# Kernel tuning notes

Hardware: AMD Instinct MI355X
Metric: run time of the kernel (lower is better)

Reference implementation:

```python
import jax, jax.numpy as jnp
import numpy as np

ALPHA = 1.0   # alpha=1 -> loss = alpha*loss_shape; temporal term weighted by (1-alpha)=0
GAMMA = 0.01  # soft-DTW smoothing
G = 0.05      # logistic weight steepness (weighted-DTW, Jeong et al. 2011)
BIG = 1e9     # finite 'infinity' (keeps vjp NaN-free vs. true inf)


def _softdtw(D, gamma):
    # Soft-DTW value of cost matrix D [N,N] via anti-diagonal (wavefront) scan.
    # R(i,j) = D[i,j] + softmin_gamma(R(i-1,j-1), R(i-1,j), R(i,j-1)),
    # R(-1,-1)=0, other out-of-range = +inf. Diagonal k holds cells (i, k-i).
    N = D.shape[-1]
    i = jnp.arange(N)

    def step(carry, k):
        r2, r1 = carry            # diagonals k-2 and k-1, indexed by row i
        j = k - i
        valid = (j >= 0) & (j < N)
        dk = jnp.where(valid, D[i, jnp.clip(j, 0, N - 1)], 0.0)
        up = jnp.where(i > 0, jnp.roll(r1, 1), BIG)     # R(i-1, j)
        left = r1                                        # R(i, j-1) (BIG where invalid)
        dg = jnp.where(i > 0, jnp.roll(r2, 1), BIG)      # R(i-1, j-1)
        dg = jnp.where((i == 0) & (j == 0), 0.0, dg)     # R(-1,-1) = 0 boundary
        smin = -gamma * jax.nn.logsumexp(jnp.stack([-dg, -up, -left]) / gamma, axis=0)
        rk = jnp.where(valid, dk + smin, BIG)
        return (r1, rk), None

    r0 = jnp.full((N,), BIG, dtype=D.dtype)
    (_, rlast), _ = jax.lax.scan(step, (r0, r0), jnp.arange(2 * N - 1))
    return rlast[N - 1]  # cell (N-1, N-1)


def _weighted_dilate(inp, tgt):
    B, N, _ = inp.shape
    idx = jnp.arange(N, dtype=inp.dtype)
    # modified-logistic weight on |i-j|, midpoint N/2, steepness g
    w = 1.0 / (1.0 + jnp.exp(-G * (jnp.abs(idx[:, None] - idx[None, :]) - N / 2.0)))
    # pairwise squared euclidean cost: D[b,i,j] = sum_d (tgt[b,i,d]-inp[b,j,d])^2
    D = jnp.sum((tgt[:, :, None, :] - inp[:, None, :, :]) ** 2, axis=-1) * w
    sdtw = jax.vmap(lambda d: _softdtw(d, GAMMA))(D)  # [B]
    loss_shape = jnp.mean(sdtw)
    return ALPHA * loss_shape  # (1-alpha)*loss_temporal == 0 at default alpha=1


def setup_inputs() -> dict:
    key = jax.random.key(0)
    k1, k2 = jax.random.split(key)
    B, N, Dm = 32, 1024, 1
    return {
        "input": jax.random.normal(k1, (B, N, Dm), dtype=jnp.float32),
        "target": jax.random.normal(k2, (B, N, Dm), dtype=jnp.float32),
    }


def reference(input, target):
    return _weighted_dilate(input, target)
```

## Files before the change

### kernel.cpp

```cpp
#include <hip/hip_runtime.h>
#include <math.h>

#define NN 1024
#define BATCH 32
#define P 8
#define NW 4
#define THREADS 256
#define DD 32
#define SW 32
#define SPAN 160
#define NT 64
#define RB 4
#define GW 0.05f
#define K2 144.2695040888963f
#define INV_K2 0.0069314718055994531f
#define BIGS 1.4426950408889634e11f

#define EXP2F(x) __builtin_amdgcn_exp2f(x)
#define LOG2F(x) __builtin_amdgcn_logf(x)

union F2U { float2 f; unsigned long long u; };

__device__ __forceinline__ float dppshr(float oldv, float src) {
    return __int_as_float(__builtin_amdgcn_update_dpp(
        __float_as_int(oldv), __float_as_int(src), 0x138, 0xF, 0xF, false));
}

__global__ __launch_bounds__(512) void ws_init(int* __restrict__ f) {
    f[threadIdx.x] = 0;
}

__global__ __launch_bounds__(THREADS) void sdtw_pipe8(
        const float* __restrict__ inp, const float* __restrict__ tgt,
        float* __restrict__ partial, int* __restrict__ flags,
        int* __restrict__ acks, unsigned long long* __restrict__ gx)
{
    __shared__ float xs[NN];
    __shared__ float wlblk[3136];
    __shared__ float2 exch[2][SPAN];

    const int bid = blockIdx.x;
    const int b = bid & 31;
    const int p = bid >> 5;
    const int tid = threadIdx.x;
    const int w = tid >> 6;
    const int lane = tid & 63;

    for (int tdx = tid; tdx < NN; tdx += THREADS) {
        xs[tdx] = inp[b * NN + tdx];
        float mO = (float)(2 * tdx + 1) - 1023.0f;
        float mE = (float)(2 * tdx) - 1023.0f;
        wlblk[544 + tdx]        = K2 / (1.0f + __expf(-GW * (fabsf(mO) - 512.0f)));
        wlblk[544 + 1024 + tdx] = K2 / (1.0f + __expf(-GW * (fabsf(mE) - 512.0f)));
    }

    const int i = 128 * p - (DD - 1) + SW * w + lane;
    const int i0 = i - lane;
    const bool rowValid = (unsigned)i < (unsigned)NN;
    int ic = min(max(i, 0), NN - 1);
    const float ti = tgt[b * NN + ic];
    const int imask = rowValid ? i : 0x3FFFFFFF;
    const float* wpBase = &wlblk[544 + 511 - i];

    float r1 = BIGS, r2 = BIGS;
    float dgp = (i == 0) ? 0.0f : BIGS;
    float bndUp = BIGS;
    float xv = 0.0f;
    int ackC = 0;

    __syncthreads();

    const int fin = b * P + p;
    const int fout = fin + 1;
    unsigned long long* gout = gx + (size_t)fout * RB * DD;
    const unsigned long long* ginb = gx + (size_t)fin * RB * DD;

    for (int t = 0; t < NT; ++t) {
        if (w == NW - 1 && p < P - 1 && t >= RB && ackC <= t - RB) {
            ackC = __hip_atomic_load(&acks[fout], __ATOMIC_RELAXED,
                                     __HIP_MEMORY_SCOPE_AGENT);
        }

        const int kbase = t << 5;
        const float* wp = wpBase + (t << 4);
        int c = kbase - 1 - i;  c = min(max(c, 0), NN - 1);
        xv = xs[c];
        int c0 = kbase - i0;    c0 = min(max(c0, 0), NN - 1);
        const float xf0 = xs[c0];
        const int jj0 = kbase - imask;

        #pragma unroll
        for (int d = 0; d < DD; ++d) {
            xv = dppshr((d == 0) ? xf0 : xv, xv);
            const float up = dppshr((d == 0) ? bndUp : r1, r1);
            const float dg = dgp;
            const float left = r1;
            const float wv = (d & 1) ? wp[1024 + ((d + 1) >> 1)]
                                     : wp[(d >> 1)];
            const float diff = ti - xv;
            const float dk = diff * diff * wv;
            const float mn = fminf(fminf(dg, up), left);
            const float md = __builtin_amdgcn_fmed3f(dg, up, left);
            const float mx = fmaxf(fmaxf(dg, up), left);
            const float s = 1.0f + EXP2F(mn - md) + EXP2F(mn - mx);
            float r = dk + mn - LOG2F(s);
            r = (jj0 >= -d) ? r : BIGS;
            r2 = r1; r1 = r; dgp = up;
        }
        if (t == NT - 1) break;

        const int buf = t & 1;
        if (lane >= DD - 1) exch[buf][SW * w + lane] = make_float2(r1, r2);
        if (w == NW - 1 && p < P - 1) {
            if (t >= RB) {
                while (ackC < t - (RB - 1)) {
                    __builtin_amdgcn_s_sleep(1);
                    ackC = __hip_atomic_load(&acks[fout], __ATOMIC_RELAXED,
                                             __HIP_MEMORY_SCOPE_AGENT);
                }
            }
            if (lane >= DD - 1 && lane < 63) {
                F2U v; v.f = make_float2(r1, r2);
                __hip_atomic_store(&gout[(size_t)(t & (RB - 1)) * DD + (lane - (DD - 1))],
                                   v.u, __ATOMIC_RELAXED, __HIP_MEMORY_SCOPE_AGENT);
            }
            asm volatile("s_waitcnt vmcnt(0)" ::: "memory");
            if (lane == 63)
                __hip_atomic_store(&flags[fout], t + 1, __ATOMIC_RELAXED,
                                   __HIP_MEMORY_SCOPE_AGENT);
        }
        __syncthreads();
        if (w > 0) {
            if (lane < DD - 1) { float2 v = exch[buf][SW * w + lane]; r1 = v.x; r2 = v.y; }
            float2 bv = exch[buf][SW * w - 1];
            float nd = dppshr(0.0f, r2);
            if (lane == 0)           { bndUp = bv.x; dgp = bv.y; }
            else if (lane <= DD - 2) dgp = nd;
        } else if (p > 0) {
            int fl;
            do {
                fl = __hip_atomic_load(&flags[fin], __ATOMIC_RELAXED,
                                       __HIP_MEMORY_SCOPE_AGENT);
                if (fl < t + 1) __builtin_amdgcn_s_sleep(1);
            } while (fl < t + 1);
            asm volatile("" ::: "memory");
            const unsigned long long* gslot = ginb + (size_t)(t & (RB - 1)) * DD;
            if (lane < DD - 1) {
                F2U v; v.u = __hip_atomic_load((unsigned long long*)&gslot[lane + 1],
                                               __ATOMIC_RELAXED, __HIP_MEMORY_SCOPE_AGENT);
                r1 = v.f.x; r2 = v.f.y;
            }
            F2U bv; bv.f = make_float2(BIGS, BIGS);
            if (lane == 0)
                bv.u = __hip_atomic_load((unsigned long long*)&gslot[0],
                                         __ATOMIC_RELAXED, __HIP_MEMORY_SCOPE_AGENT);
            float nd = dppshr(0.0f, r2);
            if (lane == 0)           { bndUp = bv.f.x; dgp = bv.f.y; }
            else if (lane <= DD - 2) dgp = nd;
            asm volatile("s_waitcnt vmcnt(0)" ::: "memory");
            if (lane == 0)
                __hip_atomic_store(&acks[fin], t + 1, __ATOMIC_RELAXED,
                                   __HIP_MEMORY_SCOPE_AGENT);
        } else {
            bndUp = BIGS;
        }
    }

    if (i == NN - 1) partial[b] = r2 * INV_K2;
}

__global__ __launch_bounds__(64) void reduce_mean32(const float* __restrict__ partial,
                                                    float* __restrict__ out) {
    float v = (threadIdx.x < BATCH) ? partial[threadIdx.x] : 0.0f;
    #pragma unroll
    for (int off = 32; off > 0; off >>= 1) v += __shfl_down(v, off);
    if (threadIdx.x == 0) out[0] = v * (1.0f / (float)BATCH);
}

extern "C" void kernel_launch(void* const* d_in, const int* in_sizes, int n_in,
                              void* d_out, int out_size, void* d_ws, size_t ws_size,
                              hipStream_t stream) {
    const float* inp = (const float*)d_in[0];
    const float* tgt = (const float*)d_in[1];
    float* out = (float*)d_out;

    float* partial = (float*)d_ws;
    int* flags = (int*)((char*)d_ws + 128);
    int* acks  = (int*)((char*)d_ws + 128 + 1024);
    unsigned long long* gx = (unsigned long long*)((char*)d_ws + 128 + 2048);

    ws_init<<<1, 512, 0, stream>>>(flags);
    sdtw_pipe8<<<BATCH * P, THREADS, 0, stream>>>(inp, tgt, partial, flags, acks, gx);
    reduce_mean32<<<1, 64, 0, stream>>>(partial, out);
}
```

Measured before the change: 229.0 us.

## Replace flag handshake with tagged payload words and prefetched cross-block boundary loads

Removes the separate per-block flag counter and instead packs a step tag into the upper 32 bits of each exchanged 64-bit word, so the consumer polls the data itself rather than a flag followed by a data load. The consumer issues its boundary loads speculatively before the block barrier and checks the tags after it. The producer's store and ack wait move to the start of the next step, and the vmcnt drains are dropped. The barrier becomes a raw s_barrier with only an LDS wait, and the ring depth shrinks from 4 to 2. This aims to take a global round trip and a memory fence off the critical wavefront path, in exchange for twice the payload traffic, a larger zero-init kernel, and more reliance on relaxed ordering being correct.

```diff
diff --git a/kernel.cpp b/kernel.cpp
--- a/kernel.cpp
+++ b/kernel.cpp
@@ -10,7 +10,7 @@
 #define SW 32
 #define SPAN 160
 #define NT 64
-#define RB 4
+#define RB 2
 #define GW 0.05f
 #define K2 144.2695040888963f
 #define INV_K2 0.0069314718055994531f
@@ -19,21 +19,27 @@
 #define EXP2F(x) __builtin_amdgcn_exp2f(x)
 #define LOG2F(x) __builtin_amdgcn_logf(x)
 
-union F2U { float2 f; unsigned long long u; };
+typedef unsigned long long u64;
 
 __device__ __forceinline__ float dppshr(float oldv, float src) {
     return __int_as_float(__builtin_amdgcn_update_dpp(
         __float_as_int(oldv), __float_as_int(src), 0x138, 0xF, 0xF, false));
 }
 
-__global__ __launch_bounds__(512) void ws_init(int* __restrict__ f) {
-    f[threadIdx.x] = 0;
+__device__ __forceinline__ u64 pk(float v, unsigned tag) {
+    return ((u64)tag << 32) | (u64)__float_as_uint(v);
+}
+
+__global__ __launch_bounds__(256) void ws_init(int* __restrict__ acks,
+                                               u64* __restrict__ gx) {
+    if (blockIdx.x == 128) acks[threadIdx.x] = 0;
+    else gx[(size_t)blockIdx.x * 256 + threadIdx.x] = 0;
 }
 
 __global__ __launch_bounds__(THREADS) void sdtw_pipe8(
         const float* __restrict__ inp, const float* __restrict__ tgt,
-        float* __restrict__ partial, int* __restrict__ flags,
-        int* __restrict__ acks, unsigned long long* __restrict__ gx)
+        float* __restrict__ partial, int* __restrict__ acks,
+        u64* __restrict__ gx)
 {
     __shared__ float xs[NN];
     __shared__ float wlblk[3136];
@@ -72,13 +78,79 @@
 
     const int fin = b * P + p;
     const int fout = fin + 1;
-    unsigned long long* gout = gx + (size_t)fout * RB * DD;
-    const unsigned long long* ginb = gx + (size_t)fin * RB * DD;
+    u64* gout = gx + (size_t)fout * (RB * DD * 2);
+    u64* ginb = gx + (size_t)fin * (RB * DD * 2);
+
+    const bool isProd = (w == NW - 1) && (p < P - 1);
+    const bool isCons = (w == 0) && (p > 0);
+
+    u64 pfA = 0, pfB = 0, pfC0 = 0, pfC1 = 0;
 
     for (int t = 0; t < NT; ++t) {
-        if (w == NW - 1 && p < P - 1 && t >= RB && ackC <= t - RB) {
-            ackC = __hip_atomic_load(&acks[fout], __ATOMIC_RELAXED,
-                                     __HIP_MEMORY_SCOPE_AGENT);
+        if (t > 0) {
+            if (isProd) {
+                if (t > RB) {
+                    while (ackC < t - RB) {
+                        __builtin_amdgcn_s_sleep(1);
+                        ackC = __hip_atomic_load(&acks[fout], __ATOMIC_RELAXED,
+                                                 __HIP_MEMORY_SCOPE_AGENT);
+                    }
+                }
+                if (lane >= DD - 1 && lane < 63) {
+                    u64* gq = gout + (size_t)((t - 1) & (RB - 1)) * (DD * 2)
+                                   + (size_t)(lane - (DD - 1)) * 2;
+                    __hip_atomic_store(&gq[0], pk(r1, (unsigned)t),
+                                       __ATOMIC_RELAXED, __HIP_MEMORY_SCOPE_AGENT);
+                    __hip_atomic_store(&gq[1], pk(r2, (unsigned)t),
+                                       __ATOMIC_RELAXED, __HIP_MEMORY_SCOPE_AGENT);
+                }
+                ackC = __hip_atomic_load(&acks[fout], __ATOMIC_RELAXED,
+                                         __HIP_MEMORY_SCOPE_AGENT);
+            }
+            if (w > 0) {
+                const int buf = (t - 1) & 1;
+                if (lane < DD - 1) { float2 v = exch[buf][SW * w + lane]; r1 = v.x; r2 = v.y; }
+                float2 bv = exch[buf][SW * w - 1];
+                float nd = dppshr(0.0f, r2);
+                if (lane == 0)           { bndUp = bv.x; dgp = bv.y; }
+                else if (lane <= DD - 2) dgp = nd;
+            } else if (p > 0) {
+                const unsigned expect = (unsigned)t;
+                const u64* gslot = ginb + (size_t)((t - 1) & (RB - 1)) * (DD * 2);
+                for (;;) {
+                    int ok = 1;
+                    if (lane < DD - 1)
+                        ok = ((unsigned)(pfA >> 32) == expect) &
+                             ((unsigned)(pfB >> 32) == expect);
+                    if (lane == 0)
+                        ok &= ((unsigned)(pfC0 >> 32) == expect) &
+                              ((unsigned)(pfC1 >> 32) == expect);
+                    if (__all(ok)) break;
+                    if (lane < DD - 1) {
+                        pfA = __hip_atomic_load((u64*)&gslot[(size_t)(lane + 1) * 2],
+                                                __ATOMIC_RELAXED, __HIP_MEMORY_SCOPE_AGENT);
+                        pfB = __hip_atomic_load((u64*)&gslot[(size_t)(lane + 1) * 2 + 1],
+                                                __ATOMIC_RELAXED, __HIP_MEMORY_SCOPE_AGENT);
+                    }
+                    if (lane == 0) {
+                        pfC0 = __hip_atomic_load((u64*)&gslot[0],
+                                                 __ATOMIC_RELAXED, __HIP_MEMORY_SCOPE_AGENT);
+                        pfC1 = __hip_atomic_load((u64*)&gslot[1],
+                                                 __ATOMIC_RELAXED, __HIP_MEMORY_SCOPE_AGENT);
+                    }
+                }
+                if (lane < DD - 1) { r1 = __uint_as_float((unsigned)pfA);
+                                     r2 = __uint_as_float((unsigned)pfB); }
+                float nd = dppshr(0.0f, r2);
+                if (lane == 0) { bndUp = __uint_as_float((unsigned)pfC0);
+                                 dgp   = __uint_as_float((unsigned)pfC1); }
+                else if (lane <= DD - 2) dgp = nd;
+                if (lane == 0)
+                    __hip_atomic_store(&acks[fin], (int)(pfC0 >> 32),
+                                       __ATOMIC_RELAXED, __HIP_MEMORY_SCOPE_AGENT);
+            } else {
+                bndUp = BIGS;
+            }
         }
 
         const int kbase = t << 5;
@@ -109,61 +181,29 @@
         }
         if (t == NT - 1) break;
 
-        const int buf = t & 1;
-        if (lane >= DD - 1) exch[buf][SW * w + lane] = make_float2(r1, r2);
-        if (w == NW - 1 && p < P - 1) {
-            if (t >= RB) {
-                while (ackC < t - (RB - 1)) {
-                    __builtin_amdgcn_s_sleep(1);
-                    ackC = __hip_atomic_load(&acks[fout], __ATOMIC_RELAXED,
-                                             __HIP_MEMORY_SCOPE_AGENT);
-                }
-            }
-            if (lane >= DD - 1 && lane < 63) {
-                F2U v; v.f = make_float2(r1, r2);
-                __hip_atomic_store(&gout[(size_t)(t & (RB - 1)) * DD + (lane - (DD - 1))],
-                                   v.u, __ATOMIC_RELAXED, __HIP_MEMORY_SCOPE_AGENT);
-            }
-            asm volatile("s_waitcnt vmcnt(0)" ::: "memory");
-            if (lane == 63)
-                __hip_atomic_store(&flags[fout], t + 1, __ATOMIC_RELAXED,
-                                   __HIP_MEMORY_SCOPE_AGENT);
+        if (w < NW - 1 && lane >= DD - 1)
+            exch[t & 1][SW * w + lane] = make_float2(r1, r2);
+
+        if (isCons) {
+            const u64* gslot = ginb + (size_t)(t & (RB - 1)) * (DD * 2);
+            if (lane < DD - 1) {
+                pfA = __hip_atomic_load((u64*)&gslot[(size_t)(lane + 1) * 2],
+                                        __ATOMIC_RELAXED, __HIP_MEMORY_SCOPE_AGENT);
+                pfB = __hip_atomic_load((u64*)&gslot[(size_t)(lane + 1) * 2 + 1],
+                                        __ATOMIC_RELAXED, __HIP_MEMORY_SCOPE_AGENT);
+            }
+            if (lane == 0) {
+                pfC0 = __hip_atomic_load((u64*)&gslot[0],
+                                         __ATOMIC_RELAXED, __HIP_MEMORY_SCOPE_AGENT);
+                pfC1 = __hip_atomic_load((u64*)&gslot[1],
+                                         __ATOMIC_RELAXED, __HIP_MEMORY_SCOPE_AGENT);
+            }
         }
-        __syncthreads();
-        if (w > 0) {
-            if (lane < DD - 1) { float2 v = exch[buf][SW * w + lane]; r1 = v.x; r2 = v.y; }
-            float2 bv = exch[buf][SW * w - 1];
-            float nd = dppshr(0.0f, r2);
-            if (lane == 0)           { bndUp = bv.x; dgp = bv.y; }
-            else if (lane <= DD - 2) dgp = nd;
-        } else if (p > 0) {
-            int fl;
-            do {
-                fl = __hip_atomic_load(&flags[fin], __ATOMIC_RELAXED,
-                                       __HIP_MEMORY_SCOPE_AGENT);
-                if (fl < t + 1) __builtin_amdgcn_s_sleep(1);
-            } while (fl < t + 1);
-            asm volatile("" ::: "memory");
-            const unsigned long long* gslot = ginb + (size_t)(t & (RB - 1)) * DD;
-            if (lane < DD - 1) {
-                F2U v; v.u = __hip_atomic_load((unsigned long long*)&gslot[lane + 1],
-                                               __ATOMIC_RELAXED, __HIP_MEMORY_SCOPE_AGENT);
-                r1 = v.f.x; r2 = v.f.y;
-            }
-            F2U bv; bv.f = make_float2(BIGS, BIGS);
-            if (lane == 0)
-                bv.u = __hip_atomic_load((unsigned long long*)&gslot[0],
-                                         __ATOMIC_RELAXED, __HIP_MEMORY_SCOPE_AGENT);
-            float nd = dppshr(0.0f, r2);
-            if (lane == 0)           { bndUp = bv.f.x; dgp = bv.f.y; }
-            else if (lane <= DD - 2) dgp = nd;
-            asm volatile("s_waitcnt vmcnt(0)" ::: "memory");
-            if (lane == 0)
-                __hip_atomic_store(&acks[fin], t + 1, __ATOMIC_RELAXED,
-                                   __HIP_MEMORY_SCOPE_AGENT);
-        } else {
-            bndUp = BIGS;
-        }
+
+        asm volatile("s_waitcnt lgkmcnt(0)" ::: "memory");
+        __builtin_amdgcn_s_barrier();
+        asm volatile("" ::: "memory");
+        __builtin_amdgcn_sched_barrier(0);
     }
 
     if (i == NN - 1) partial[b] = r2 * INV_K2;
@@ -185,11 +225,10 @@
     float* out = (float*)d_out;
 
     float* partial = (float*)d_ws;
-    int* flags = (int*)((char*)d_ws + 128);
-    int* acks  = (int*)((char*)d_ws + 128 + 1024);
-    unsigned long long* gx = (unsigned long long*)((char*)d_ws + 128 + 2048);
-
-    ws_init<<<1, 512, 0, stream>>>(flags);
-    sdtw_pipe8<<<BATCH * P, THREADS, 0, stream>>>(inp, tgt, partial, flags, acks, gx);
+    int* acks  = (int*)((char*)d_ws + 128);
+    u64* gx    = (u64*)((char*)d_ws + 2048);
+
+    ws_init<<<129, 256, 0, stream>>>(acks, gx);
+    sdtw_pipe8<<<BATCH * P, THREADS, 0, stream>>>(inp, tgt, partial, acks, gx);
     reduce_mean32<<<1, 64, 0, stream>>>(partial, out);
 }
```

Result: faster. 216.7 us (-5.3%).
